# Performance work log

Measured on AMD Instinct MI355X. Metric: run time of the kernel, lower is better.

The kernel has to match this reference:

```python
import jax, jax.numpy as jnp
import numpy as np

B, L, H, NT = 16, 2048, 512, 8
HEAD_H = max(32, H // 2)
OUT = 2 * H + NT
LN_EPS = 1e-5


def setup_inputs() -> dict:
    key = jax.random.key(0)
    ks = jax.random.split(key, 32)
    def w(i, shape):
        fan_in = shape[0] if len(shape) > 1 else shape[0]
        return jax.random.normal(ks[i], shape, jnp.float32) / np.sqrt(fan_in)
    z = lambda shape: jnp.zeros(shape, jnp.float32)
    return {
        "x": jax.random.normal(ks[0], (B, L, 2), jnp.float32),
        "t": jax.random.uniform(ks[1], (B, L, 1), jnp.float32),
        "Wt1": w(2, (1, NT)), "bt1": z((NT,)),
        "Wt2": w(3, (NT, NT)), "bt2": z((NT,)),
        "Wpf": w(4, (2 + NT, H)), "bpf": z((H,)),
        "Wpb": w(5, (2 + NT, H)), "bpb": z((H,)),
        "Wzf": w(6, (H, H)), "bzf": z((H,)),
        "Whf": w(7, (H, H)), "bhf": z((H,)),
        "Wzb": w(8, (H, H)), "bzb": z((H,)),
        "Whb": w(9, (H, H)), "bhb": z((H,)),
        "ln_g": jnp.ones((OUT,), jnp.float32), "ln_b": z((OUT,)),
        "time_scale": jnp.array(5.0, jnp.float32),
        "Wg1": w(10, (OUT, HEAD_H)), "bg1": z((HEAD_H,)),
        "Wg2": w(11, (HEAD_H, 1)), "bg2": z((1,)),
    }


def _mingru_states(xc, Wp, bp, Wz, bz, Wh, bh):
    """Run minGRU over xc (B,L,D); return h_prev states: out[:,ti] = h before step ti."""
    inp = xc @ Wp + bp                      # (B,L,H)
    zg = jax.nn.sigmoid(inp @ Wz + bz)
    h_tilde = jnp.tanh(inp @ Wh + bh)
    a = 1.0 - zg                            # decay
    b = zg * h_tilde                        # input injection
    def step(h, ab):
        h = ab[0] * h + ab[1]
        return h, h
    h0 = jnp.zeros((xc.shape[0], Wh.shape[1]), xc.dtype)
    _, hs = jax.lax.scan(step, h0, (jnp.moveaxis(a, 1, 0), jnp.moveaxis(b, 1, 0)))
    hs = jnp.moveaxis(hs, 0, 1)             # (B,L,H), hs[:,ti] = h after step ti
    # Original stores h_prev at each position -> shift right with zero prefix.
    return jnp.concatenate([jnp.zeros_like(hs[:, :1]), hs[:, :-1]], axis=1)


def reference(x, t, Wt1, bt1, Wt2, bt2, Wpf, bpf, Wpb, bpb,
              Wzf, bzf, Whf, bhf, Wzb, bzb, Whb, bhb,
              ln_g, ln_b, time_scale, Wg1, bg1, Wg2, bg2):
    t_enc = jnp.maximum(t @ Wt1 + bt1, 0.0) @ Wt2 + bt2   # (B,L,NT)
    xc = jnp.concatenate([x, t_enc], axis=-1)              # (B,L,2+NT)
    h_fwd = _mingru_states(xc, Wpf, bpf, Wzf, bzf, Whf, bhf)
    # Backward direction: run scan on time-reversed input, then flip back.
    h_bwd = _mingru_states(xc[:, ::-1], Wpb, bpb, Wzb, bzb, Whb, bhb)[:, ::-1]
    h_bi = jnp.concatenate([h_fwd, h_bwd, t_enc], axis=-1)  # (B,L,OUT)
    mu = jnp.mean(h_bi, axis=-1, keepdims=True)
    var = jnp.mean(jnp.square(h_bi - mu), axis=-1, keepdims=True)
    h_bi = (h_bi - mu) * jax.lax.rsqrt(var + LN_EPS) * ln_g + ln_b
    h_bi = jnp.concatenate([h_bi[..., :-NT], h_bi[..., -NT:] * time_scale], axis=-1)
    hid = jax.nn.gelu(h_bi @ Wg1 + bg1, approximate=False)
    return hid @ Wg2 + bg2                                  # (B,L,1)
```

## Files before the change

### kernel.cpp

```cpp
#include <hip/hip_runtime.h>
#include <hip/hip_bf16.h>
#include <math.h>

#define B_    16
#define L_    2048
#define H_    512
#define NT_   8
#define OUT_  1032
#define KPAD_ 1056
#define HEAD_ 256
#define CH_   16
#define CL_   (L_/CH_)
#define NW_   1024

#define ACH_  136
#define ASTR_ (ACH_*8)
#define RB5_  32

typedef short bf16x8 __attribute__((ext_vector_type(8)));
typedef float f32x4  __attribute__((ext_vector_type(4)));

__device__ __forceinline__ float b2f(unsigned short u) {
    union { unsigned int u32; float f; } v; v.u32 = ((unsigned int)u) << 16; return v.f;
}
__device__ __forceinline__ unsigned short f2b(float f) {
    __hip_bfloat16 h = __float2bfloat16(f);
    return *reinterpret_cast<unsigned short*>(&h);
}
__device__ __forceinline__ float sigmoid_f(float x) {
    return 1.f / (1.f + exp2f(-1.44269504f * x));
}
__device__ __forceinline__ float tanh_f(float x) {
    float e = exp2f(2.88539008f * x);
    return 1.f - 2.f / (e + 1.f);
}
__device__ __forceinline__ float gelu_f(float g) {
    float u  = 0.70710678118654752f * g;
    float ax = fabsf(u);
    float t  = 1.f / (1.f + 0.3275911f * ax);
    float poly = ((((1.061405429f*t - 1.453152027f)*t + 1.421413741f)*t
                   - 0.284496736f)*t + 0.254829592f)*t;
    float e  = exp2f(-1.44269504f * ax * ax);
    float er = 1.f - poly * e;
    er = (u < 0.f) ? -er : er;
    return 0.5f * g * (1.f + er);
}

__global__ __launch_bounds__(256) void kT(const float* __restrict__ in,
                                          unsigned short* __restrict__ out,
                                          int R, int C, int RP)
{
    __shared__ float tile[32][33];
    int c0 = blockIdx.x * 32, r0 = blockIdx.y * 32;
    int tx = threadIdx.x & 31, ty = threadIdx.x >> 5;
    #pragma unroll
    for (int j = 0; j < 32; j += 8) {
        int r = r0 + ty + j, c = c0 + tx;
        tile[ty + j][tx] = (r < R && c < C) ? in[(size_t)r*C + c] : 0.f;
    }
    __syncthreads();
    #pragma unroll
    for (int j = 0; j < 32; j += 8) {
        int c = c0 + ty + j, r = r0 + tx;
        if (c < C && r < RP) out[(size_t)c*RP + r] = f2b(tile[tx][ty + j]);
    }
}

__global__ __launch_bounds__(256) void kP(const float* __restrict__ Wg1,
                                          uint4* __restrict__ P)
{
    int idx = blockIdx.x*256 + threadIdx.x;
    if (idx >= 33*1024) return;
    int kb = idx >> 10;
    int rem = idx & 1023;
    int c  = rem >> 2;
    int kg = rem & 3;
    int k0 = kb*32 + kg*8;
    unsigned short o[8];
    #pragma unroll
    for (int j = 0; j < 8; j++) {
        int k = k0 + j;
        o[j] = (k < OUT_) ? f2b(Wg1[(size_t)k*HEAD_ + c]) : (unsigned short)0;
    }
    P[idx] = *(const uint4*)o;
}

__global__ __launch_bounds__(256) void k1_tenc_inp(
    const float* __restrict__ x, const float* __restrict__ t,
    const float* __restrict__ Wt1, const float* __restrict__ bt1,
    const float* __restrict__ Wt2, const float* __restrict__ bt2,
    const float* __restrict__ Wp, const float* __restrict__ bp,
    float* __restrict__ t_enc,
    unsigned short* __restrict__ inp)
{
    int wv = threadIdx.x >> 6, lane = threadIdx.x & 63;
    size_t row = (size_t)blockIdx.x*4 + wv;
    float tv = t[row];
    float r1[NT_], te[NT_];
    #pragma unroll
    for (int k = 0; k < NT_; k++) r1[k] = fmaxf(tv*Wt1[k] + bt1[k], 0.f);
    #pragma unroll
    for (int j = 0; j < NT_; j++) {
        float a = bt2[j];
        #pragma unroll
        for (int k = 0; k < NT_; k++) a = fmaf(r1[k], Wt2[k*NT_+j], a);
        te[j] = a;
    }
    if (lane < NT_) t_enc[row*NT_ + lane] = te[lane];
    float x0 = x[row*2+0], x1 = x[row*2+1];
    int c0 = lane*8;
    float af[8];
    #pragma unroll
    for (int j = 0; j < 8; j++) {
        int c = c0 + j;
        af[j] = fmaf(x0, Wp[c], fmaf(x1, Wp[H_+c], bp[c]));
    }
    #pragma unroll
    for (int k = 0; k < NT_; k++) {
        #pragma unroll
        for (int j = 0; j < 8; j++)
            af[j] = fmaf(te[k], Wp[(2+k)*H_+c0+j], af[j]);
    }
    unsigned short of[8];
    #pragma unroll
    for (int j = 0; j < 8; j++) of[j] = f2b(af[j]);
    *(uint4*)&inp[row*H_ + c0] = *(const uint4*)of;
}

__global__ __launch_bounds__(256) void k3g(
    const unsigned short* __restrict__ inp,
    const unsigned short* __restrict__ WT,
    unsigned short* __restrict__ zt_out,
    int nwg)
{
    __shared__ __align__(16) unsigned short As[128*40];
    __shared__ __align__(16) unsigned short Bs[128*40];
    int tid = threadIdx.x;
    int lane = tid & 63, w = tid >> 6;
    int wm = w >> 1, wn = w & 1;
    int kg = lane >> 4, lr = lane & 15;

    int bid = blockIdx.x;
    int cpx = nwg >> 3;
    int tile = (bid & 7) * cpx + (bid >> 3);
    int row0 = (tile >> 3) * 128;
    int n0   = (tile & 7) * 128;

    f32x4 acc[4][4];
    #pragma unroll
    for (int m = 0; m < 4; m++)
        #pragma unroll
        for (int n = 0; n < 4; n++) acc[m][n] = (f32x4){0.f,0.f,0.f,0.f};

    int ar = tid >> 1, aseg = tid & 1;

    uint4 va0, va1, vb0, vb1;
    {
        const uint4* ga = (const uint4*)&inp[(size_t)(row0+ar)*H_ + aseg*16];
        va0 = ga[0]; va1 = ga[1];
        const uint4* gb = (const uint4*)&WT[(size_t)(n0+ar)*H_ + aseg*16];
        vb0 = gb[0]; vb1 = gb[1];
    }

    for (int k0 = 0; k0 < H_; k0 += 32) {
        __syncthreads();
        *(uint4*)&As[ar*40 + aseg*16]     = va0;
        *(uint4*)&As[ar*40 + aseg*16 + 8] = va1;
        *(uint4*)&Bs[ar*40 + aseg*16]     = vb0;
        *(uint4*)&Bs[ar*40 + aseg*16 + 8] = vb1;
        __syncthreads();
        if (k0 + 32 < H_) {
            const uint4* ga = (const uint4*)&inp[(size_t)(row0+ar)*H_ + k0+32 + aseg*16];
            va0 = ga[0]; va1 = ga[1];
            const uint4* gb = (const uint4*)&WT[(size_t)(n0+ar)*H_ + k0+32 + aseg*16];
            vb0 = gb[0]; vb1 = gb[1];
        }
        bf16x8 af[4], bf[4];
        #pragma unroll
        for (int m = 0; m < 4; m++)
            af[m] = *(const bf16x8*)&As[(wm*64 + m*16 + lr)*40 + kg*8];
        #pragma unroll
        for (int n = 0; n < 4; n++)
            bf[n] = *(const bf16x8*)&Bs[(wn*64 + n*16 + lr)*40 + kg*8];
        #pragma unroll
        for (int m = 0; m < 4; m++)
            #pragma unroll
            for (int n = 0; n < 4; n++)
                acc[m][n] = __builtin_amdgcn_mfma_f32_16x16x32_bf16(af[m], bf[n], acc[m][n], 0, 0, 0);
    }

    #pragma unroll
    for (int m = 0; m < 4; m++)
        #pragma unroll
        for (int n = 0; n < 4; n++) {
            int colg = n0 + wn*64 + n*16 + lr;
            #pragma unroll
            for (int r = 0; r < 4; r++) {
                int rowg = row0 + wm*64 + m*16 + kg*4 + r;
                zt_out[(size_t)rowg*NW_ + colg] = f2b(acc[m][n][r]);
            }
        }
}

__global__ __launch_bounds__(256) void k4a(
    unsigned short* __restrict__ ATF, unsigned short* __restrict__ ATB,
    const float* __restrict__ bzf, const float* __restrict__ bhf,
    const float* __restrict__ bzb, const float* __restrict__ bhb,
    float* __restrict__ Scar, float* __restrict__ Pcar, int nb)
{
    int g = blockIdx.x*256 + threadIdx.x;
    int col   = g & (H_-1);
    int chunk = (g >> 9) & (CH_-1);
    int rest  = g >> 13;
    int bb    = rest % nb;
    int dir   = rest / nb;
    unsigned short* AT = dir ? ATB : ATF;
    float bzv = (dir ? bzb : bzf)[col];
    float bhv = (dir ? bhb : bhf)[col];
    size_t base = (size_t)bb * L_ * NW_ + col;
    float h = 0.f, pp = 1.f;
    if (dir == 0) {
        int lo = chunk * CL_;
        for (int p = 0; p < CL_; p += 8) {
            unsigned short zv[8], hv[8];
            #pragma unroll
            for (int j = 0; j < 8; j++) {
                size_t idx = base + (size_t)(lo+p+j)*NW_;
                zv[j] = AT[idx]; hv[j] = AT[idx + H_];
            }
            #pragma unroll
            for (int j = 0; j < 8; j++) {
                size_t idx = base + (size_t)(lo+p+j)*NW_;
                float zg = sigmoid_f(b2f(zv[j]) + bzv);
                float a  = 1.f - zg;
                float bg = zg * tanh_f(b2f(hv[j]) + bhv);
                AT[idx]      = f2b(h);
                AT[idx + H_] = f2b(pp);
                h = fmaf(a, h, bg);
                pp *= a;
            }
        }
    } else {
        int hi = chunk * CL_ + CL_ - 1;
        for (int p = 0; p < CL_; p += 8) {
            unsigned short zv[8], hv[8];
            #pragma unroll
            for (int j = 0; j < 8; j++) {
                size_t idx = base + (size_t)(hi-p-j)*NW_;
                zv[j] = AT[idx]; hv[j] = AT[idx + H_];
            }
            #pragma unroll
            for (int j = 0; j < 8; j++) {
                size_t idx = base + (size_t)(hi-p-j)*NW_;
                float zg = sigmoid_f(b2f(zv[j]) + bzv);
                float a  = 1.f - zg;
                float bg = zg * tanh_f(b2f(hv[j]) + bhv);
                AT[idx]      = f2b(h);
                AT[idx + H_] = f2b(pp);
                h = fmaf(a, h, bg);
                pp *= a;
            }
        }
    }
    int ci = ((dir*nb + bb)*CH_ + chunk)*H_ + col;
    Scar[ci] = h; Pcar[ci] = pp;
}

__global__ __launch_bounds__(256) void k4b(
    const float* __restrict__ Scar, const float* __restrict__ Pcar,
    float* __restrict__ Hstart, int nb)
{
    int g = blockIdx.x*256 + threadIdx.x;
    int col  = g & (H_-1);
    int rest = g >> 9;
    int bb   = rest % nb;
    int dir  = rest / nb;
    int baseci = (dir*nb + bb)*CH_;
    float h = 0.f;
    if (dir == 0) {
        for (int c = 0; c < CH_; c++) {
            int ci = (baseci + c)*H_ + col;
            Hstart[ci] = h;
            h = Scar[ci] + Pcar[ci]*h;
        }
    } else {
        for (int c = CH_-1; c >= 0; c--) {
            int ci = (baseci + c)*H_ + col;
            Hstart[ci] = h;
            h = Scar[ci] + Pcar[ci]*h;
        }
    }
}

__global__ __launch_bounds__(256) void k5_fused(
    const unsigned short* __restrict__ ATF, const unsigned short* __restrict__ ATB,
    const float* __restrict__ Hstart,
    const float* __restrict__ tenc,
    const float* __restrict__ ln_g, const float* __restrict__ ln_b,
    const float* __restrict__ tsp,
    const uint4* __restrict__ P,
    const float* __restrict__ bg1, const float* __restrict__ Wg2,
    const float* __restrict__ bg2,
    float* __restrict__ out, int nb)
{
    __shared__ __align__(16) unsigned short A[RB5_*ASTR_];
    __shared__ float red[4][RB5_];
    int tid = threadIdx.x, lane = tid & 63, wv = tid >> 6;
    int kg = lane >> 4, lr = lane & 15;
    int row0 = blockIdx.x * RB5_;
    float ts = tsp[0];

    int bb    = row0 >> 11;
    int chunk = (row0 & (L_-1)) >> 7;
    int cif = ((bb)*CH_ + chunk)*H_;
    int cib = ((nb + bb)*CH_ + chunk)*H_;
    int c0 = lane*8;
    float4 hfa = *(const float4*)&Hstart[cif + c0];
    float4 hfb = *(const float4*)&Hstart[cif + c0 + 4];
    float4 hba = *(const float4*)&Hstart[cib + c0];
    float4 hbb = *(const float4*)&Hstart[cib + c0 + 4];
    float h0f[8] = {hfa.x,hfa.y,hfa.z,hfa.w,hfb.x,hfb.y,hfb.z,hfb.w};
    float h0b[8] = {hba.x,hba.y,hba.z,hba.w,hbb.x,hbb.y,hbb.z,hbb.w};

    uint4 SF[8], PF[8], SB[8], PB[8];
    float tvv[8];
    #pragma unroll
    for (int i = 0; i < 8; i++) {
        size_t row = (size_t)row0 + wv*8 + i;
        SF[i] = *(const uint4*)&ATF[row*NW_ + c0];
        PF[i] = *(const uint4*)&ATF[row*NW_ + H_ + c0];
        SB[i] = *(const uint4*)&ATB[row*NW_ + c0];
        PB[i] = *(const uint4*)&ATB[row*NW_ + H_ + c0];
    }
    #pragma unroll
    for (int i = 0; i < 8; i++) {
        size_t row = (size_t)row0 + wv*8 + i;
        tvv[i] = (lane < NT_) ? tenc[row*NT_ + lane] : 0.f;
    }

    float gf[8], bf_[8], gb_[8], bb_[8];
    #pragma unroll
    for (int j = 0; j < 8; j++) {
        gf[j]  = ln_g[c0+j];     bf_[j] = ln_b[c0+j];
        gb_[j] = ln_g[H_+c0+j];  bb_[j] = ln_b[H_+c0+j];
    }
    float gt = 0.f, bt = 0.f;
    if (lane < NT_) { gt = ln_g[2*H_+lane]; bt = ln_b[2*H_+lane]; }

    #pragma unroll
    for (int i = 0; i < 8; i++) {
        int r = wv*8 + i;
        const unsigned short* sf = (const unsigned short*)&SF[i];
        const unsigned short* pf = (const unsigned short*)&PF[i];
        const unsigned short* sb = (const unsigned short*)&SB[i];
        const unsigned short* pb = (const unsigned short*)&PB[i];
        float fv[8], bv[8];
        float S = 0.f, Q = 0.f;
        #pragma unroll
        for (int j = 0; j < 8; j++) {
            fv[j] = fmaf(b2f(pf[j]), h0f[j], b2f(sf[j]));
            S += fv[j]; Q += fv[j]*fv[j];
            bv[j] = fmaf(b2f(pb[j]), h0b[j], b2f(sb[j]));
            S += bv[j]; Q += bv[j]*bv[j];
        }
        float tv = tvv[i];
        S += tv; Q += tv*tv;
        #pragma unroll
        for (int off = 32; off > 0; off >>= 1) {
            S += __shfl_xor(S, off, 64);
            Q += __shfl_xor(Q, off, 64);
        }
        float mu = S * (1.f/1032.f);
        float rs = rsqrtf(Q * (1.f/1032.f) - mu*mu + 1e-5f);
        int key = r & 7;
        unsigned short o[8];
        #pragma unroll
        for (int j = 0; j < 8; j++) o[j] = f2b((fv[j]-mu)*rs*gf[j] + bf_[j]);
        *(uint4*)&A[r*ASTR_ + ((lane ^ key)*8)] = *(const uint4*)o;
        #pragma unroll
        for (int j = 0; j < 8; j++) o[j] = f2b((bv[j]-mu)*rs*gb_[j] + bb_[j]);
        *(uint4*)&A[r*ASTR_ + (((64+lane) ^ key)*8)] = *(const uint4*)o;
        if (lane < NT_) {
            A[r*ASTR_ + ((128 ^ key)*8) + lane] =
                f2b(((tv-mu)*rs*gt + bt) * ts);
        } else if (lane < 32) {
            int byte = 2064 + 2*(lane-8);
            int cc = byte >> 4, rem = (byte & 15) >> 1;
            A[r*ASTR_ + ((cc ^ key)*8) + rem] = 0;
        }
    }
    __syncthreads();

    f32x4 acc[2][4];
    #pragma unroll
    for (int m = 0; m < 2; m++)
        #pragma unroll
        for (int n = 0; n < 4; n++) acc[m][n] = (f32x4){0.f,0.f,0.f,0.f};

    const uint4* Pw = P + wv*256 + lr*4 + kg;
    int keyA = lr & 7;

#define LOADB(v0,v1,v2,v3,KB) do { \
        const uint4* q_ = Pw + (KB)*1024; \
        v0 = *(const bf16x8*)&q_[0]; \
        v1 = *(const bf16x8*)&q_[64]; \
        v2 = *(const bf16x8*)&q_[128]; \
        v3 = *(const bf16x8*)&q_[192]; \
    } while(0)
#define LDSA0(KB) (*(const bf16x8*)&A[lr*ASTR_      + ((((KB)*4+kg) ^ keyA)*8)])
#define LDSA1(KB) (*(const bf16x8*)&A[(16+lr)*ASTR_ + ((((KB)*4+kg) ^ keyA)*8)])
#define MFMA8(v0,v1,v2,v3,a0_,a1_) do { \
        acc[0][0] = __builtin_amdgcn_mfma_f32_16x16x32_bf16(a0_, v0, acc[0][0],0,0,0); \
        acc[0][1] = __builtin_amdgcn_mfma_f32_16x16x32_bf16(a0_, v1, acc[0][1],0,0,0); \
        acc[0][2] = __builtin_amdgcn_mfma_f32_16x16x32_bf16(a0_, v2, acc[0][2],0,0,0); \
        acc[0][3] = __builtin_amdgcn_mfma_f32_16x16x32_bf16(a0_, v3, acc[0][3],0,0,0); \
        acc[1][0] = __builtin_amdgcn_mfma_f32_16x16x32_bf16(a1_, v0, acc[1][0],0,0,0); \
        acc[1][1] = __builtin_amdgcn_mfma_f32_16x16x32_bf16(a1_, v1, acc[1][1],0,0,0); \
        acc[1][2] = __builtin_amdgcn_mfma_f32_16x16x32_bf16(a1_, v2, acc[1][2],0,0,0); \
        acc[1][3] = __builtin_amdgcn_mfma_f32_16x16x32_bf16(a1_, v3, acc[1][3],0,0,0); \
    } while(0)

    bf16x8 a0,a1,a2,a3, d0,d1,d2,d3;
    LOADB(a0,a1,a2,a3, 0);
    for (int kb = 0; kb < 32; kb += 2) {
        LOADB(d0,d1,d2,d3, kb+1);
        bf16x8 af0 = LDSA0(kb), af1 = LDSA1(kb);
        MFMA8(a0,a1,a2,a3, af0, af1);
        LOADB(a0,a1,a2,a3, kb+2);
        af0 = LDSA0(kb+1); af1 = LDSA1(kb+1);
        MFMA8(d0,d1,d2,d3, af0, af1);
    }
    {
        bf16x8 af0 = LDSA0(32), af1 = LDSA1(32);
        MFMA8(a0,a1,a2,a3, af0, af1);
    }
#undef LOADB
#undef LDSA0
#undef LDSA1
#undef MFMA8

    float rsum[2][4] = {{0.f,0.f,0.f,0.f},{0.f,0.f,0.f,0.f}};
    #pragma unroll
    for (int n = 0; n < 4; n++) {
        int colg = wv*64 + n*16 + lr;
        float bgv = bg1[colg], w2v = Wg2[colg];
        #pragma unroll
        for (int m = 0; m < 2; m++)
            #pragma unroll
            for (int r = 0; r < 4; r++) {
                float gv = gelu_f(acc[m][n][r] + bgv);
                rsum[m][r] = fmaf(gv, w2v, rsum[m][r]);
            }
    }
    #pragma unroll
    for (int off = 1; off < 16; off <<= 1)
        #pragma unroll
        for (int m = 0; m < 2; m++)
            #pragma unroll
            for (int r = 0; r < 4; r++)
                rsum[m][r] += __shfl_xor(rsum[m][r], off, 64);
    if (lr == 0) {
        #pragma unroll
        for (int m = 0; m < 2; m++)
            #pragma unroll
            for (int r = 0; r < 4; r++)
                red[wv][m*16 + kg*4 + r] = rsum[m][r];
    }
    __syncthreads();
    if (tid < RB5_)
        out[row0 + tid] = red[0][tid] + red[1][tid] + red[2][tid] + red[3][tid] + bg2[0];
}

extern "C" void kernel_launch(void* const* d_in, const int* in_sizes, int n_in,
                              void* d_out, int out_size, void* d_ws, size_t ws_size,
                              hipStream_t stream)
{
    const float* x    = (const float*)d_in[0];
    const float* t    = (const float*)d_in[1];
    const float* Wt1  = (const float*)d_in[2];
    const float* bt1  = (const float*)d_in[3];
    const float* Wt2  = (const float*)d_in[4];
    const float* bt2  = (const float*)d_in[5];
    const float* Wpf  = (const float*)d_in[6];
    const float* bpf  = (const float*)d_in[7];
    const float* Wpb  = (const float*)d_in[8];
    const float* bpb  = (const float*)d_in[9];
    const float* Wzf  = (const float*)d_in[10];
    const float* bzf  = (const float*)d_in[11];
    const float* Whf  = (const float*)d_in[12];
    const float* bhf  = (const float*)d_in[13];
    const float* Wzb  = (const float*)d_in[14];
    const float* bzb  = (const float*)d_in[15];
    const float* Whb  = (const float*)d_in[16];
    const float* bhb  = (const float*)d_in[17];
    const float* ln_g = (const float*)d_in[18];
    const float* ln_b = (const float*)d_in[19];
    const float* tsc  = (const float*)d_in[20];
    const float* Wg1  = (const float*)d_in[21];
    const float* bg1  = (const float*)d_in[22];
    const float* Wg2  = (const float*)d_in[23];
    const float* bg2  = (const float*)d_in[24];
    float* out = (float*)d_out;

    char* p = (char*)d_ws;
    auto carve = [&](size_t bytes) -> char* {
        char* q = p; p += (bytes + 255) & ~(size_t)255; return q;
    };

    unsigned short* WTf = (unsigned short*)carve((size_t)2*H_*H_*2);
    unsigned short* WTb = (unsigned short*)carve((size_t)2*H_*H_*2);
    uint4*          Pg  = (uint4*)carve((size_t)33*1024*16);

    const size_t perBatch = (size_t)L_*H_*2
                          + (size_t)L_*NW_*2*2
                          + (size_t)L_*NT_*4
                          + (size_t)CH_*H_*4*3*2;
    size_t fixedUsed = (size_t)(p - (char*)d_ws) + 64*1024;
    int NB = B_;
    while (NB > 1 && fixedUsed + (size_t)NB*perBatch > ws_size) NB >>= 1;

    unsigned short* inp = (unsigned short*)carve((size_t)NB*L_*H_*2);
    unsigned short* ATF = (unsigned short*)carve((size_t)NB*L_*NW_*2);
    unsigned short* ATB = (unsigned short*)carve((size_t)NB*L_*NW_*2);
    float* tenc   = (float*)carve((size_t)NB*L_*NT_*4);
    float* Scar   = (float*)carve((size_t)2*NB*CH_*H_*4);
    float* Pcar   = (float*)carve((size_t)2*NB*CH_*H_*4);
    float* Hstart = (float*)carve((size_t)2*NB*CH_*H_*4);

    {
        dim3 g(H_/32, H_/32);
        kT<<<g, 256, 0, stream>>>(Wzf, WTf,            H_, H_, H_);
        kT<<<g, 256, 0, stream>>>(Whf, WTf + H_*H_,    H_, H_, H_);
        kT<<<g, 256, 0, stream>>>(Wzb, WTb,            H_, H_, H_);
        kT<<<g, 256, 0, stream>>>(Whb, WTb + H_*H_,    H_, H_, H_);
        kP<<<132, 256, 0, stream>>>(Wg1, Pg);
    }

    for (int b0 = 0; b0 < B_; b0 += NB) {
        int rows = NB * L_;
        int nwg3 = (rows/128) * 8;

        k1_tenc_inp<<<rows/4, 256, 0, stream>>>(
            x + (size_t)b0*L_*2, t + (size_t)b0*L_,
            Wt1, bt1, Wt2, bt2, Wpf, bpf, tenc, inp);
        k3g<<<nwg3, 256, 0, stream>>>(inp, WTf, ATF, nwg3);

        k1_tenc_inp<<<rows/4, 256, 0, stream>>>(
            x + (size_t)b0*L_*2, t + (size_t)b0*L_,
            Wt1, bt1, Wt2, bt2, Wpb, bpb, tenc, inp);
        k3g<<<nwg3, 256, 0, stream>>>(inp, WTb, ATB, nwg3);

        int scanThreads = 2*NB*H_*CH_;
        k4a<<<scanThreads/256, 256, 0, stream>>>(ATF, ATB, bzf, bhf, bzb, bhb,
                                                 Scar, Pcar, NB);
        k4b<<<(2*NB*H_)/256, 256, 0, stream>>>(Scar, Pcar, Hstart, NB);

        k5_fused<<<rows/RB5_, 256, 0, stream>>>(
            ATF, ATB, Hstart, tenc, ln_g, ln_b, tsc,
            Pg, bg1, Wg2, bg2, out + (size_t)b0*L_, NB);
    }
}
```

Baseline: 309.0 us.

## Split fused LayerNorm+head kernel into LN pass and tiled MFMA head GEMM

The fused k5 kernel, which did LayerNorm into shared memory and then a 32-row head GEMM streaming Wg1 from global, is split in two. k5a_ln normalises each row and writes bf16 results in place into the ATF buffer, whose row stride grows to 1152 so the 1032 features plus padding fit. k5b_head is a 64-row tiled GEMM that stages both A and the packed Wg1 in LDS with register prefetch, plus a grouped block order. This increases B reuse per block, but adds a global round trip for the normalized activations and one extra launch.

After: 378.6 us. 22.5% more time.

```diff
diff --git a/kernel.cpp b/kernel.cpp
--- a/kernel.cpp
+++ b/kernel.cpp
@@ -7,15 +7,11 @@
 #define H_    512
 #define NT_   8
 #define OUT_  1032
-#define KPAD_ 1056
 #define HEAD_ 256
 #define CH_   16
 #define CL_   (L_/CH_)
-#define NW_   1024
-
-#define ACH_  136
-#define ASTR_ (ACH_*8)
-#define RB5_  32
+#define NWS_  1152
+#define KP2_  1088
 
 typedef short bf16x8 __attribute__((ext_vector_type(8)));
 typedef float f32x4  __attribute__((ext_vector_type(4)));
@@ -70,7 +66,7 @@
                                           uint4* __restrict__ P)
 {
     int idx = blockIdx.x*256 + threadIdx.x;
-    if (idx >= 33*1024) return;
+    if (idx >= 34*1024) return;
     int kb = idx >> 10;
     int rem = idx & 1023;
     int c  = rem >> 2;
@@ -197,7 +193,7 @@
             #pragma unroll
             for (int r = 0; r < 4; r++) {
                 int rowg = row0 + wm*64 + m*16 + kg*4 + r;
-                zt_out[(size_t)rowg*NW_ + colg] = f2b(acc[m][n][r]);
+                zt_out[(size_t)rowg*NWS_ + colg] = f2b(acc[m][n][r]);
             }
         }
 }
@@ -217,7 +213,7 @@
     unsigned short* AT = dir ? ATB : ATF;
     float bzv = (dir ? bzb : bzf)[col];
     float bhv = (dir ? bhb : bhf)[col];
-    size_t base = (size_t)bb * L_ * NW_ + col;
+    size_t base = (size_t)bb * L_ * NWS_ + col;
     float h = 0.f, pp = 1.f;
     if (dir == 0) {
         int lo = chunk * CL_;
@@ -225,12 +221,12 @@
             unsigned short zv[8], hv[8];
             #pragma unroll
             for (int j = 0; j < 8; j++) {
-                size_t idx = base + (size_t)(lo+p+j)*NW_;
+                size_t idx = base + (size_t)(lo+p+j)*NWS_;
                 zv[j] = AT[idx]; hv[j] = AT[idx + H_];
             }
             #pragma unroll
             for (int j = 0; j < 8; j++) {
-                size_t idx = base + (size_t)(lo+p+j)*NW_;
+                size_t idx = base + (size_t)(lo+p+j)*NWS_;
                 float zg = sigmoid_f(b2f(zv[j]) + bzv);
                 float a  = 1.f - zg;
                 float bg = zg * tanh_f(b2f(hv[j]) + bhv);
@@ -246,12 +242,12 @@
             unsigned short zv[8], hv[8];
             #pragma unroll
             for (int j = 0; j < 8; j++) {
-                size_t idx = base + (size_t)(hi-p-j)*NW_;
+                size_t idx = base + (size_t)(hi-p-j)*NWS_;
                 zv[j] = AT[idx]; hv[j] = AT[idx + H_];
             }
             #pragma unroll
             for (int j = 0; j < 8; j++) {
-                size_t idx = base + (size_t)(hi-p-j)*NW_;
+                size_t idx = base + (size_t)(hi-p-j)*NWS_;
                 float zg = sigmoid_f(b2f(zv[j]) + bzv);
                 float a  = 1.f - zg;
                 float bg = zg * tanh_f(b2f(hv[j]) + bhv);
@@ -292,157 +288,145 @@
     }
 }
 
-__global__ __launch_bounds__(256) void k5_fused(
-    const unsigned short* __restrict__ ATF, const unsigned short* __restrict__ ATB,
-    const float* __restrict__ Hstart,
-    const float* __restrict__ tenc,
+__global__ __launch_bounds__(256) void k5a_ln(
+    unsigned short* __restrict__ ATF, const unsigned short* __restrict__ ATB,
+    const float* __restrict__ Hstart, const float* __restrict__ tenc,
     const float* __restrict__ ln_g, const float* __restrict__ ln_b,
-    const float* __restrict__ tsp,
-    const uint4* __restrict__ P,
-    const float* __restrict__ bg1, const float* __restrict__ Wg2,
-    const float* __restrict__ bg2,
-    float* __restrict__ out, int nb)
-{
-    __shared__ __align__(16) unsigned short A[RB5_*ASTR_];
-    __shared__ float red[4][RB5_];
-    int tid = threadIdx.x, lane = tid & 63, wv = tid >> 6;
-    int kg = lane >> 4, lr = lane & 15;
-    int row0 = blockIdx.x * RB5_;
-    float ts = tsp[0];
-
-    int bb    = row0 >> 11;
-    int chunk = (row0 & (L_-1)) >> 7;
-    int cif = ((bb)*CH_ + chunk)*H_;
+    const float* __restrict__ tsp, int nb)
+{
+    int wv = threadIdx.x >> 6, lane = threadIdx.x & 63;
+    size_t row = (size_t)blockIdx.x*4 + wv;
+    int bb    = (int)(row >> 11);
+    int chunk = ((int)row & (L_-1)) >> 7;
+    int cif = (bb*CH_ + chunk)*H_;
     int cib = ((nb + bb)*CH_ + chunk)*H_;
     int c0 = lane*8;
+    float ts = tsp[0];
+
+    size_t rb = row * NWS_;
+    uint4 SF = *(const uint4*)&ATF[rb + c0];
+    uint4 PF = *(const uint4*)&ATF[rb + H_ + c0];
+    uint4 SB = *(const uint4*)&ATB[rb + c0];
+    uint4 PB = *(const uint4*)&ATB[rb + H_ + c0];
     float4 hfa = *(const float4*)&Hstart[cif + c0];
     float4 hfb = *(const float4*)&Hstart[cif + c0 + 4];
     float4 hba = *(const float4*)&Hstart[cib + c0];
     float4 hbb = *(const float4*)&Hstart[cib + c0 + 4];
     float h0f[8] = {hfa.x,hfa.y,hfa.z,hfa.w,hfb.x,hfb.y,hfb.z,hfb.w};
     float h0b[8] = {hba.x,hba.y,hba.z,hba.w,hbb.x,hbb.y,hbb.z,hbb.w};
-
-    uint4 SF[8], PF[8], SB[8], PB[8];
-    float tvv[8];
-    #pragma unroll
-    for (int i = 0; i < 8; i++) {
-        size_t row = (size_t)row0 + wv*8 + i;
-        SF[i] = *(const uint4*)&ATF[row*NW_ + c0];
-        PF[i] = *(const uint4*)&ATF[row*NW_ + H_ + c0];
-        SB[i] = *(const uint4*)&ATB[row*NW_ + c0];
-        PB[i] = *(const uint4*)&ATB[row*NW_ + H_ + c0];
-    }
-    #pragma unroll
-    for (int i = 0; i < 8; i++) {
-        size_t row = (size_t)row0 + wv*8 + i;
-        tvv[i] = (lane < NT_) ? tenc[row*NT_ + lane] : 0.f;
-    }
-
-    float gf[8], bf_[8], gb_[8], bb_[8];
+    const unsigned short* sf = (const unsigned short*)&SF;
+    const unsigned short* pf = (const unsigned short*)&PF;
+    const unsigned short* sb = (const unsigned short*)&SB;
+    const unsigned short* pb = (const unsigned short*)&PB;
+
+    float fv[8], bv[8];
+    float S = 0.f, Q = 0.f;
     #pragma unroll
     for (int j = 0; j < 8; j++) {
-        gf[j]  = ln_g[c0+j];     bf_[j] = ln_b[c0+j];
-        gb_[j] = ln_g[H_+c0+j];  bb_[j] = ln_b[H_+c0+j];
-    }
-    float gt = 0.f, bt = 0.f;
-    if (lane < NT_) { gt = ln_g[2*H_+lane]; bt = ln_b[2*H_+lane]; }
-
-    #pragma unroll
-    for (int i = 0; i < 8; i++) {
-        int r = wv*8 + i;
-        const unsigned short* sf = (const unsigned short*)&SF[i];
-        const unsigned short* pf = (const unsigned short*)&PF[i];
-        const unsigned short* sb = (const unsigned short*)&SB[i];
-        const unsigned short* pb = (const unsigned short*)&PB[i];
-        float fv[8], bv[8];
-        float S = 0.f, Q = 0.f;
+        fv[j] = fmaf(b2f(pf[j]), h0f[j], b2f(sf[j]));
+        S += fv[j]; Q += fv[j]*fv[j];
+        bv[j] = fmaf(b2f(pb[j]), h0b[j], b2f(sb[j]));
+        S += bv[j]; Q += bv[j]*bv[j];
+    }
+    float tv = 0.f;
+    if (lane < NT_) { tv = tenc[row*NT_ + lane]; S += tv; Q += tv*tv; }
+    #pragma unroll
+    for (int off = 32; off > 0; off >>= 1) {
+        S += __shfl_xor(S, off, 64);
+        Q += __shfl_xor(Q, off, 64);
+    }
+    float mu = S * (1.f/1032.f);
+    float rs = rsqrtf(Q * (1.f/1032.f) - mu*mu + 1e-5f);
+
+    unsigned short o[8];
+    #pragma unroll
+    for (int j = 0; j < 8; j++)
+        o[j] = f2b((fv[j]-mu)*rs*ln_g[c0+j] + ln_b[c0+j]);
+    *(uint4*)&ATF[rb + c0] = *(const uint4*)o;
+    #pragma unroll
+    for (int j = 0; j < 8; j++)
+        o[j] = f2b((bv[j]-mu)*rs*ln_g[H_+c0+j] + ln_b[H_+c0+j]);
+    *(uint4*)&ATF[rb + H_ + c0] = *(const uint4*)o;
+    if (lane < NT_) {
+        int c = 2*H_ + lane;
+        ATF[rb + 1024 + lane] = f2b(((tv-mu)*rs*ln_g[c] + ln_b[c]) * ts);
+    } else {
+        ATF[rb + 1024 + lane] = 0;
+    }
+}
+
+__global__ __launch_bounds__(256, 2) void k5b_head(
+    const unsigned short* __restrict__ hbi,
+    const uint4* __restrict__ P,
+    const float* __restrict__ bg1, const float* __restrict__ Wg2,
+    const float* __restrict__ bg2,
+    float* __restrict__ out, int nwg)
+{
+    __shared__ __align__(16) unsigned short As[64*68];
+    __shared__ __align__(16) uint4 Bs[2048];
+    __shared__ float red[2][64];
+    int tid = threadIdx.x, lane = tid & 63, w = tid >> 6;
+    int wm = w >> 1, wn = w & 1;
+    int lr = lane & 15, kg = lane >> 4;
+
+    int bid = blockIdx.x;
+    int cpx = nwg >> 3;
+    int tile = (bid & 7) * cpx + (bid >> 3);
+    int row0 = tile * 64;
+
+    f32x4 acc[2][8];
+    #pragma unroll
+    for (int m = 0; m < 2; m++)
+        #pragma unroll
+        for (int n = 0; n < 8; n++) acc[m][n] = (f32x4){0.f,0.f,0.f,0.f};
+
+    int arow = tid & 63, ac8 = tid >> 6;
+    const unsigned short* asrc = &hbi[(size_t)(row0 + arow)*NWS_];
+
+    uint4 va0, va1, vb[8];
+    va0 = *(const uint4*)&asrc[ac8*8];
+    va1 = *(const uint4*)&asrc[(ac8+4)*8];
+    #pragma unroll
+    for (int j = 0; j < 8; j++) vb[j] = P[tid*8 + j];
+
+    for (int step = 0; step < 17; step++) {
+        __syncthreads();
+        *(uint4*)&As[arow*68 + ac8*8]     = va0;
+        *(uint4*)&As[arow*68 + (ac8+4)*8] = va1;
         #pragma unroll
         for (int j = 0; j < 8; j++) {
-            fv[j] = fmaf(b2f(pf[j]), h0f[j], b2f(sf[j]));
-            S += fv[j]; Q += fv[j]*fv[j];
-            bv[j] = fmaf(b2f(pb[j]), h0b[j], b2f(sb[j]));
-            S += bv[j]; Q += bv[j]*bv[j];
-        }
-        float tv = tvv[i];
-        S += tv; Q += tv*tv;
-        #pragma unroll
-        for (int off = 32; off > 0; off >>= 1) {
-            S += __shfl_xor(S, off, 64);
-            Q += __shfl_xor(Q, off, 64);
-        }
-        float mu = S * (1.f/1032.f);
-        float rs = rsqrtf(Q * (1.f/1032.f) - mu*mu + 1e-5f);
-        int key = r & 7;
-        unsigned short o[8];
-        #pragma unroll
-        for (int j = 0; j < 8; j++) o[j] = f2b((fv[j]-mu)*rs*gf[j] + bf_[j]);
-        *(uint4*)&A[r*ASTR_ + ((lane ^ key)*8)] = *(const uint4*)o;
-        #pragma unroll
-        for (int j = 0; j < 8; j++) o[j] = f2b((bv[j]-mu)*rs*gb_[j] + bb_[j]);
-        *(uint4*)&A[r*ASTR_ + (((64+lane) ^ key)*8)] = *(const uint4*)o;
-        if (lane < NT_) {
-            A[r*ASTR_ + ((128 ^ key)*8) + lane] =
-                f2b(((tv-mu)*rs*gt + bt) * ts);
-        } else if (lane < 32) {
-            int byte = 2064 + 2*(lane-8);
-            int cc = byte >> 4, rem = (byte & 15) >> 1;
-            A[r*ASTR_ + ((cc ^ key)*8) + rem] = 0;
-        }
-    }
-    __syncthreads();
-
-    f32x4 acc[2][4];
-    #pragma unroll
-    for (int m = 0; m < 2; m++)
-        #pragma unroll
-        for (int n = 0; n < 4; n++) acc[m][n] = (f32x4){0.f,0.f,0.f,0.f};
-
-    const uint4* Pw = P + wv*256 + lr*4 + kg;
-    int keyA = lr & 7;
-
-#define LOADB(v0,v1,v2,v3,KB) do { \
-        const uint4* q_ = Pw + (KB)*1024; \
-        v0 = *(const bf16x8*)&q_[0]; \
-        v1 = *(const bf16x8*)&q_[64]; \
-        v2 = *(const bf16x8*)&q_[128]; \
-        v3 = *(const bf16x8*)&q_[192]; \
-    } while(0)
-#define LDSA0(KB) (*(const bf16x8*)&A[lr*ASTR_      + ((((KB)*4+kg) ^ keyA)*8)])
-#define LDSA1(KB) (*(const bf16x8*)&A[(16+lr)*ASTR_ + ((((KB)*4+kg) ^ keyA)*8)])
-#define MFMA8(v0,v1,v2,v3,a0_,a1_) do { \
-        acc[0][0] = __builtin_amdgcn_mfma_f32_16x16x32_bf16(a0_, v0, acc[0][0],0,0,0); \
-        acc[0][1] = __builtin_amdgcn_mfma_f32_16x16x32_bf16(a0_, v1, acc[0][1],0,0,0); \
-        acc[0][2] = __builtin_amdgcn_mfma_f32_16x16x32_bf16(a0_, v2, acc[0][2],0,0,0); \
-        acc[0][3] = __builtin_amdgcn_mfma_f32_16x16x32_bf16(a0_, v3, acc[0][3],0,0,0); \
-        acc[1][0] = __builtin_amdgcn_mfma_f32_16x16x32_bf16(a1_, v0, acc[1][0],0,0,0); \
-        acc[1][1] = __builtin_amdgcn_mfma_f32_16x16x32_bf16(a1_, v1, acc[1][1],0,0,0); \
-        acc[1][2] = __builtin_amdgcn_mfma_f32_16x16x32_bf16(a1_, v2, acc[1][2],0,0,0); \
-        acc[1][3] = __builtin_amdgcn_mfma_f32_16x16x32_bf16(a1_, v3, acc[1][3],0,0,0); \
-    } while(0)
-
-    bf16x8 a0,a1,a2,a3, d0,d1,d2,d3;
-    LOADB(a0,a1,a2,a3, 0);
-    for (int kb = 0; kb < 32; kb += 2) {
-        LOADB(d0,d1,d2,d3, kb+1);
-        bf16x8 af0 = LDSA0(kb), af1 = LDSA1(kb);
-        MFMA8(a0,a1,a2,a3, af0, af1);
-        LOADB(a0,a1,a2,a3, kb+2);
-        af0 = LDSA0(kb+1); af1 = LDSA1(kb+1);
-        MFMA8(d0,d1,d2,d3, af0, af1);
-    }
-    {
-        bf16x8 af0 = LDSA0(32), af1 = LDSA1(32);
-        MFMA8(a0,a1,a2,a3, af0, af1);
-    }
-#undef LOADB
-#undef LDSA0
-#undef LDSA1
-#undef MFMA8
+            int i = tid*8 + j;
+            int kbl = (i >> 10) & 1;
+            int c   = (i & 1023) >> 2;
+            int kgw = i & 3;
+            Bs[kbl*1024 + (c>>4)*64 + kgw*16 + (c&15)] = vb[j];
+        }
+        __syncthreads();
+        if (step < 16) {
+            int k0 = (step+1)*64;
+            va0 = *(const uint4*)&asrc[k0 + ac8*8];
+            va1 = *(const uint4*)&asrc[k0 + (ac8+4)*8];
+            const uint4* ps = P + (step+1)*2048 + tid*8;
+            #pragma unroll
+            for (int j = 0; j < 8; j++) vb[j] = ps[j];
+        }
+        #pragma unroll
+        for (int kk = 0; kk < 2; kk++) {
+            bf16x8 af0 = *(const bf16x8*)&As[(wm*32 + lr)*68      + (kk*4+kg)*8];
+            bf16x8 af1 = *(const bf16x8*)&As[(wm*32 + 16 + lr)*68 + (kk*4+kg)*8];
+            #pragma unroll
+            for (int n = 0; n < 8; n++) {
+                bf16x8 bf = *(const bf16x8*)&Bs[kk*1024 + (wn*8+n)*64 + lane];
+                acc[0][n] = __builtin_amdgcn_mfma_f32_16x16x32_bf16(af0, bf, acc[0][n], 0, 0, 0);
+                acc[1][n] = __builtin_amdgcn_mfma_f32_16x16x32_bf16(af1, bf, acc[1][n], 0, 0, 0);
+            }
+        }
+    }
 
     float rsum[2][4] = {{0.f,0.f,0.f,0.f},{0.f,0.f,0.f,0.f}};
     #pragma unroll
-    for (int n = 0; n < 4; n++) {
-        int colg = wv*64 + n*16 + lr;
+    for (int n = 0; n < 8; n++) {
+        int colg = wn*128 + n*16 + lr;
         float bgv = bg1[colg], w2v = Wg2[colg];
         #pragma unroll
         for (int m = 0; m < 2; m++)
@@ -464,11 +448,11 @@
         for (int m = 0; m < 2; m++)
             #pragma unroll
             for (int r = 0; r < 4; r++)
-                red[wv][m*16 + kg*4 + r] = rsum[m][r];
+                red[wn][wm*32 + m*16 + kg*4 + r] = rsum[m][r];
     }
     __syncthreads();
-    if (tid < RB5_)
-        out[row0 + tid] = red[0][tid] + red[1][tid] + red[2][tid] + red[3][tid] + bg2[0];
+    if (tid < 64)
+        out[row0 + tid] = red[0][tid] + red[1][tid] + bg2[0];
 }
 
 extern "C" void kernel_launch(void* const* d_in, const int* in_sizes, int n_in,
@@ -509,10 +493,10 @@
 
     unsigned short* WTf = (unsigned short*)carve((size_t)2*H_*H_*2);
     unsigned short* WTb = (unsigned short*)carve((size_t)2*H_*H_*2);
-    uint4*          Pg  = (uint4*)carve((size_t)33*1024*16);
+    uint4*          Pg  = (uint4*)carve((size_t)34*1024*16);
 
     const size_t perBatch = (size_t)L_*H_*2
-                          + (size_t)L_*NW_*2*2
+                          + (size_t)L_*NWS_*2*2
                           + (size_t)L_*NT_*4
                           + (size_t)CH_*H_*4*3*2;
     size_t fixedUsed = (size_t)(p - (char*)d_ws) + 64*1024;
@@ -520,8 +504,8 @@
     while (NB > 1 && fixedUsed + (size_t)NB*perBatch > ws_size) NB >>= 1;
 
     unsigned short* inp = (unsigned short*)carve((size_t)NB*L_*H_*2);
-    unsigned short* ATF = (unsigned short*)carve((size_t)NB*L_*NW_*2);
-    unsigned short* ATB = (unsigned short*)carve((size_t)NB*L_*NW_*2);
+    unsigned short* ATF = (unsigned short*)carve((size_t)NB*L_*NWS_*2);
+    unsigned short* ATB = (unsigned short*)carve((size_t)NB*L_*NWS_*2);
     float* tenc   = (float*)carve((size_t)NB*L_*NT_*4);
     float* Scar   = (float*)carve((size_t)2*NB*CH_*H_*4);
     float* Pcar   = (float*)carve((size_t)2*NB*CH_*H_*4);
@@ -529,11 +513,11 @@
 
     {
         dim3 g(H_/32, H_/32);
-        kT<<<g, 256, 0, stream>>>(Wzf, WTf,            H_, H_, H_);
-        kT<<<g, 256, 0, stream>>>(Whf, WTf + H_*H_,    H_, H_, H_);
-        kT<<<g, 256, 0, stream>>>(Wzb, WTb,            H_, H_, H_);
-        kT<<<g, 256, 0, stream>>>(Whb, WTb + H_*H_,    H_, H_, H_);
-        kP<<<132, 256, 0, stream>>>(Wg1, Pg);
+        kT<<<g, 256, 0, stream>>>(Wzf, WTf,         H_, H_, H_);
+        kT<<<g, 256, 0, stream>>>(Whf, WTf + H_*H_, H_, H_, H_);
+        kT<<<g, 256, 0, stream>>>(Wzb, WTb,         H_, H_, H_);
+        kT<<<g, 256, 0, stream>>>(Whb, WTb + H_*H_, H_, H_, H_);
+        kP<<<136, 256, 0, stream>>>(Wg1, Pg);
     }
 
     for (int b0 = 0; b0 < B_; b0 += NB) {
@@ -555,8 +539,11 @@
                                                  Scar, Pcar, NB);
         k4b<<<(2*NB*H_)/256, 256, 0, stream>>>(Scar, Pcar, Hstart, NB);
 
-        k5_fused<<<rows/RB5_, 256, 0, stream>>>(
-            ATF, ATB, Hstart, tenc, ln_g, ln_b, tsc,
-            Pg, bg1, Wg2, bg2, out + (size_t)b0*L_, NB);
-    }
-}
+        k5a_ln<<<rows/4, 256, 0, stream>>>(ATF, ATB, Hstart, tenc,
+                                           ln_g, ln_b, tsc, NB);
+
+        int nwg5 = rows/64;
+        k5b_head<<<nwg5, 256, 0, stream>>>(ATF, Pg, bg1, Wg2, bg2,
+                                           out + (size_t)b0*L_, nwg5);
+    }
+}
```
